# Kernel optimization log

Measured on AMD Instinct MI355X. Metric: run time of the kernel, lower is better.

## Reference

```python
import jax, jax.numpy as jnp
import numpy as np

E = 1024  # dim_model
H = 16    # num_heads
HD = E // H
B, S = 32, 2048
LN_EPS = 1e-5


def setup_inputs() -> dict:
    key = jax.random.key(0)
    ks = jax.random.split(key, 8)
    x = jax.random.normal(ks[0], (B, S, E), dtype=jnp.float32)
    key_padding_mask = jax.random.randint(ks[1], (B, S), 0, 2).astype(jnp.int32)
    # learned seed (xavier_uniform over [1,1,E])
    bound = float(np.sqrt(6.0 / (1 + E)))
    seed = jax.random.uniform(ks[2], (1, 1, E), minval=-bound, maxval=bound, dtype=jnp.float32)
    # MHA params: packed in_proj [3E, E] (q,k,v stacked) + bias, out_proj [E,E]+bias
    w_scale = 1.0 / np.sqrt(E)
    in_proj_w = jax.random.uniform(ks[3], (3 * E, E), minval=-w_scale, maxval=w_scale, dtype=jnp.float32)
    in_proj_b = jnp.zeros((3 * E,), dtype=jnp.float32)
    out_w = jax.random.uniform(ks[4], (E, E), minval=-w_scale, maxval=w_scale, dtype=jnp.float32)
    out_b = jnp.zeros((E,), dtype=jnp.float32)
    ln_g = jnp.ones((E,), dtype=jnp.float32)
    ln_b = jnp.zeros((E,), dtype=jnp.float32)
    return {"x": x, "key_padding_mask": key_padding_mask, "seed": seed,
            "in_proj_w": in_proj_w, "in_proj_b": in_proj_b,
            "out_w": out_w, "out_b": out_b, "ln_g": ln_g, "ln_b": ln_b}


def reference(x, key_padding_mask, seed, in_proj_w, in_proj_b, out_w, out_b, ln_g, ln_b):
    wq, wk, wv = in_proj_w[:E], in_proj_w[E:2 * E], in_proj_w[2 * E:]
    bq, bk, bv = in_proj_b[:E], in_proj_b[E:2 * E], in_proj_b[2 * E:]
    # q from single learned seed: [1,1,E] -> [1,H,1,HD] (broadcast over batch)
    q = (seed @ wq.T + bq).reshape(1, 1, H, HD).transpose(0, 2, 1, 3)
    k = (x @ wk.T + bk).reshape(x.shape[0], -1, H, HD).transpose(0, 2, 1, 3)  # [B,H,S,HD]
    v = (x @ wv.T + bv).reshape(x.shape[0], -1, H, HD).transpose(0, 2, 1, 3)
    scale = 1.0 / jnp.sqrt(jnp.asarray(HD, dtype=x.dtype))
    scores = jnp.einsum('bhqd,bhkd->bhqk', q * scale, k)  # broadcasts q batch dim -> [B,H,1,S]
    pad = (key_padding_mask == 0)[:, None, None, :]  # True = pad
    scores = jnp.where(pad, -jnp.inf, scores)
    attn = jax.nn.softmax(scores, axis=-1)
    ctx = jnp.einsum('bhqk,bhkd->bhqd', attn, v)  # [B,H,1,HD]
    ctx = ctx.transpose(0, 2, 1, 3).reshape(x.shape[0], E)  # squeeze single query
    out = ctx @ out_w.T + out_b
    mu = jnp.mean(out, axis=-1, keepdims=True)
    var = jnp.mean(jnp.square(out - mu), axis=-1, keepdims=True)
    return (out - mu) / jnp.sqrt(var + LN_EPS) * ln_g + ln_b
```

## Files before the change

kernel.cpp:

```cpp
#include <hip/hip_runtime.h>
#include <hip/hip_bf16.h>
#include <math.h>

#define E 1024
#define H 16
#define HD 64
#define B 32
#define S 2048
#define CH 16
#define CTOK (S / CH)
#define SUB 32
#define NSUB (CTOK / SUB)
#define BHE (B * H * E)

typedef __attribute__((ext_vector_type(8))) short short8;
typedef __attribute__((ext_vector_type(4))) float f32x4;

__device__ __forceinline__ short f2bf(float f) {
    union { __hip_bfloat16 h; short s; } u;
    u.h = __float2bfloat16(f);
    return u.s;
}
__device__ __forceinline__ unsigned pack_bf2(float x, float y) {
    unsigned ux = (__float_as_uint(x) + 0x8000u) >> 16;
    unsigned uy = (__float_as_uint(y) + 0x8000u) & 0xffff0000u;
    return uy | ux;
}

__global__ __launch_bounds__(256) void qproj_kernel(const float* __restrict__ W,
                                                    const float* __restrict__ bqkv,
                                                    const float* __restrict__ seed,
                                                    float* __restrict__ q) {
    int gw = (blockIdx.x * 256 + threadIdx.x) >> 6;
    int lane = threadIdx.x & 63;
    if (gw >= E) return;
    const float4* row = (const float4*)(W + (size_t)gw * E);
    const float4* sd = (const float4*)seed;
    float acc = 0.f;
#pragma unroll
    for (int k = 0; k < 4; ++k) {
        float4 w4 = row[k * 64 + lane];
        float4 s4 = sd[k * 64 + lane];
        acc = fmaf(w4.x, s4.x, acc); acc = fmaf(w4.y, s4.y, acc);
        acc = fmaf(w4.z, s4.z, acc); acc = fmaf(w4.w, s4.w, acc);
    }
#pragma unroll
    for (int off = 32; off > 0; off >>= 1) acc += __shfl_down(acc, off, 64);
    if (lane == 0) q[gw] = acc + bqkv[gw];
}

__global__ __launch_bounds__(256) void uproj_kernel(const float* __restrict__ W,
                                                    const float* __restrict__ q,
                                                    short* __restrict__ ubf) {
    int h = blockIdx.y;
    int e = blockIdx.x * 256 + threadIdx.x;
    __shared__ float qs[HD];
    if (threadIdx.x < HD) qs[threadIdx.x] = q[h * HD + threadIdx.x];
    __syncthreads();
    const float* Wk = W + ((size_t)(E + h * HD)) * E + e;
    float acc = 0.f;
#pragma unroll 8
    for (int d = 0; d < HD; ++d) acc = fmaf(qs[d], Wk[(size_t)d * E], acc);
    ubf[(size_t)h * E + e] = f2bf(acc * 0.125f);
}

__global__ __launch_bounds__(512, 4) void fused_kernel(const float* __restrict__ x,
                                                       const int* __restrict__ mask,
                                                       const short* __restrict__ ubf,
                                                       unsigned* __restrict__ partu,
                                                       float* __restrict__ mstat,
                                                       float* __restrict__ lstat) {
    int ss = blockIdx.x, b = blockIdx.y;
    __shared__ short xB[SUB * E];
    __shared__ float scp[8 * 64 * 4];
    __shared__ float pcur[SUB * H];
    __shared__ int   mk[CTOK];
    __shared__ float mrun[H], lrun[H], rfac[H];
    __shared__ float wred[8][16];

    int tid = threadIdx.x, lane = tid & 63, wid = tid >> 6;

    if (tid < H) { mrun[tid] = -1e30f; lrun[tid] = 0.f; }
    for (int i = tid; i < CTOK; i += 512) mk[i] = mask[(size_t)b * S + ss * CTOK + i];

    float4 a4[8];
#pragma unroll
    for (int h = 0; h < 8; ++h) a4[h] = make_float4(0.f, 0.f, 0.f, 0.f);

    int pe4 = tid & 255, phg = tid >> 8;

    __syncthreads();

    for (int sub = 0; sub < NSUB; ++sub) {
        int t0 = sub * SUB;

        {
            int tok = tid >> 4;
            int es  = tid & 15;
            const float* xr = x + ((size_t)b * S + ss * CTOK + t0 + tok) * E;
            bool live = mk[t0 + tok] != 0;
#pragma unroll
            for (int i = 0; i < 8; ++i) {
                int e0 = (es + i * 16) * 8;
                if (live) {
                    float4 lo = *(const float4*)(xr + e0);
                    float4 hi = *(const float4*)(xr + e0 + 4);
                    short8 v;
                    v[0] = f2bf(lo.x); v[1] = f2bf(lo.y); v[2] = f2bf(lo.z); v[3] = f2bf(lo.w);
                    v[4] = f2bf(hi.x); v[5] = f2bf(hi.y); v[6] = f2bf(hi.z); v[7] = f2bf(hi.w);
                    int byte = (tok * 2048 + e0 * 2) ^ ((tok & 7) << 4);
                    *(short8*)((char*)xB + byte) = v;
                }
            }
        }
        __syncthreads();

        {
            int tw = wid & 1, kq = wid >> 1;
            int tr = lane & 15, kg = lane >> 4;
            int tok = tw * 16 + tr;
            f32x4 acc = {0.f, 0.f, 0.f, 0.f};
            const short* ub = ubf + (size_t)tr * E;
#pragma unroll
            for (int st = 0; st < 8; ++st) {
                int e0 = kq * 256 + st * 32 + kg * 8;
                int byte = (tok * 2048 + e0 * 2) ^ ((tok & 7) << 4);
                short8 a = *(const short8*)((char*)xB + byte);
                short8 bv = *(const short8*)(ub + e0);
                acc = __builtin_amdgcn_mfma_f32_16x16x32_bf16(a, bv, acc, 0, 0, 0);
            }
            *(f32x4*)&scp[(wid * 64 + lane) * 4] = acc;
        }
        __syncthreads();

        {
            int tok = tid >> 4, h = tid & 15;
            int tw = tok >> 4, r = tok & 3, kg2 = (tok & 15) >> 2;
            float s = 0.f;
#pragma unroll
            for (int kq = 0; kq < 4; ++kq)
                s += scp[((kq * 2 + tw) * 64 + kg2 * 16 + h) * 4 + r];
            bool live = mk[t0 + tok] != 0;
            float sv = live ? s : -1e30f;
            float mx = sv;
            mx = fmaxf(mx, __shfl_xor(mx, 16, 64));
            mx = fmaxf(mx, __shfl_xor(mx, 32, 64));
            if (lane < 16) wred[wid][lane] = mx;
            __syncthreads();
            if (tid < 16) {
                float mt = wred[0][tid];
#pragma unroll
                for (int w = 1; w < 8; ++w) mt = fmaxf(mt, wred[w][tid]);
                float mo = mrun[tid];
                float mn = fmaxf(mo, mt);
                rfac[tid] = __expf(mo - mn);
                mrun[tid] = mn;
            }
            __syncthreads();
            float p = live ? __expf(s - mrun[h]) : 0.f;
            pcur[tok * 16 + h] = p;
            float ps = p;
            ps += __shfl_xor(ps, 16, 64);
            ps += __shfl_xor(ps, 32, 64);
            if (lane < 16) wred[wid][lane] = ps;
            __syncthreads();
            if (tid < 16) {
                float lt = 0.f;
#pragma unroll
                for (int w = 0; w < 8; ++w) lt += wred[w][tid];
                lrun[tid] = lrun[tid] * rfac[tid] + lt;
            }
        }
        __syncthreads();

        {
            const float* rf = rfac + phg * 8;
#pragma unroll
            for (int h = 0; h < 8; ++h) {
                float r = rf[h];
                a4[h].x *= r; a4[h].y *= r; a4[h].z *= r; a4[h].w *= r;
            }
            int ebyte = pe4 * 8;
            for (int tok = 0; tok < SUB; ++tok) {
                if (!mk[t0 + tok]) continue;
                int byte = (tok * 2048 + ebyte) ^ ((tok & 7) << 4);
                uint2 xv = *(const uint2*)((char*)xB + byte);
                float xe0 = __uint_as_float(xv.x << 16);
                float xe1 = __uint_as_float(xv.x & 0xffff0000u);
                float xe2 = __uint_as_float(xv.y << 16);
                float xe3 = __uint_as_float(xv.y & 0xffff0000u);
                float4 p0 = *(const float4*)&pcur[tok * 16 + phg * 8];
                float4 p1 = *(const float4*)&pcur[tok * 16 + phg * 8 + 4];
                a4[0].x = fmaf(p0.x, xe0, a4[0].x); a4[0].y = fmaf(p0.x, xe1, a4[0].y);
                a4[0].z = fmaf(p0.x, xe2, a4[0].z); a4[0].w = fmaf(p0.x, xe3, a4[0].w);
                a4[1].x = fmaf(p0.y, xe0, a4[1].x); a4[1].y = fmaf(p0.y, xe1, a4[1].y);
                a4[1].z = fmaf(p0.y, xe2, a4[1].z); a4[1].w = fmaf(p0.y, xe3, a4[1].w);
                a4[2].x = fmaf(p0.z, xe0, a4[2].x); a4[2].y = fmaf(p0.z, xe1, a4[2].y);
                a4[2].z = fmaf(p0.z, xe2, a4[2].z); a4[2].w = fmaf(p0.z, xe3, a4[2].w);
                a4[3].x = fmaf(p0.w, xe0, a4[3].x); a4[3].y = fmaf(p0.w, xe1, a4[3].y);
                a4[3].z = fmaf(p0.w, xe2, a4[3].z); a4[3].w = fmaf(p0.w, xe3, a4[3].w);
                a4[4].x = fmaf(p1.x, xe0, a4[4].x); a4[4].y = fmaf(p1.x, xe1, a4[4].y);
                a4[4].z = fmaf(p1.x, xe2, a4[4].z); a4[4].w = fmaf(p1.x, xe3, a4[4].w);
                a4[5].x = fmaf(p1.y, xe0, a4[5].x); a4[5].y = fmaf(p1.y, xe1, a4[5].y);
                a4[5].z = fmaf(p1.y, xe2, a4[5].z); a4[5].w = fmaf(p1.y, xe3, a4[5].w);
                a4[6].x = fmaf(p1.z, xe0, a4[6].x); a4[6].y = fmaf(p1.z, xe1, a4[6].y);
                a4[6].z = fmaf(p1.z, xe2, a4[6].z); a4[6].w = fmaf(p1.z, xe3, a4[6].w);
                a4[7].x = fmaf(p1.w, xe0, a4[7].x); a4[7].y = fmaf(p1.w, xe1, a4[7].y);
                a4[7].z = fmaf(p1.w, xe2, a4[7].z); a4[7].w = fmaf(p1.w, xe3, a4[7].w);
            }
        }
        __syncthreads();
    }

    unsigned* pb = partu + ((size_t)ss * B + b) * (H * E / 2) + pe4 * 2;
#pragma unroll
    for (int h = 0; h < 8; ++h) {
        uint2 v;
        v.x = pack_bf2(a4[h].x, a4[h].y);
        v.y = pack_bf2(a4[h].z, a4[h].w);
        *(uint2*)&pb[(size_t)(phg * 8 + h) * (E / 2)] = v;
    }
    if (tid < 16) {
        mstat[((size_t)ss * B + b) * H + tid] = mrun[tid];
        lstat[((size_t)ss * B + b) * H + tid] = lrun[tid];
    }
}

__global__ __launch_bounds__(256) void ctxc_kernel(const float* __restrict__ W,
                                                   const float* __restrict__ bqkv,
                                                   const unsigned* __restrict__ partu,
                                                   const float* __restrict__ mstat,
                                                   const float* __restrict__ lstat,
                                                   float* __restrict__ ctx) {
    int cb = blockIdx.x, b = blockIdx.y, t = threadIdx.x;
    int h0 = cb * 4;
    __shared__ float xls[4 * E];
    __shared__ float fs[4][CH];
    __shared__ float linv[4];
    if (t < 4) {
        int h = h0 + t;
        float mv[CH];
        float mg = -1e30f;
#pragma unroll
        for (int c = 0; c < CH; ++c) {
            mv[c] = mstat[((size_t)c * B + b) * H + h];
            mg = fmaxf(mg, mv[c]);
        }
        float l = 0.f;
#pragma unroll
        for (int c = 0; c < CH; ++c) {
            float fc = __expf(mv[c] - mg);
            fs[t][c] = fc;
            l = fmaf(fc, lstat[((size_t)c * B + b) * H + h], l);
        }
        linv[t] = 1.f / l;
    }
    __syncthreads();
    for (int i = t; i < 4 * E / 2; i += 256) {
        int hl = i >> 9, e2 = i & 511;
        float sx = 0.f, sy = 0.f;
#pragma unroll 4
        for (int c = 0; c < CH; ++c) {
            float fc = fs[hl][c];
            unsigned v = partu[(((size_t)c * B + b) * H + h0 + hl) * (E / 2) + e2];
            sx = fmaf(fc, __uint_as_float(v << 16), sx);
            sy = fmaf(fc, __uint_as_float(v & 0xffff0000u), sy);
        }
        float li = linv[hl];
        xls[hl * E + e2 * 2] = sx * li;
        xls[hl * E + e2 * 2 + 1] = sy * li;
    }
    __syncthreads();
    int c = cb * 256 + t;
    int h = c >> 6;
    const float4* wr = (const float4*)(W + ((size_t)(2 * E + c)) * E);
    const float4* xl = (const float4*)(xls + (h - h0) * E);
    float acc = bqkv[2 * E + c];
#pragma unroll 4
    for (int e4 = 0; e4 < E / 4; ++e4) {
        float4 w = wr[e4], xv = xl[e4];
        acc = fmaf(w.x, xv.x, acc); acc = fmaf(w.y, xv.y, acc);
        acc = fmaf(w.z, xv.z, acc); acc = fmaf(w.w, xv.w, acc);
    }
    ctx[(size_t)b * E + c] = acc;
}

__global__ __launch_bounds__(256) void outproj_kernel(const float* __restrict__ Wo,
                                                      const float* __restrict__ ob,
                                                      const float* __restrict__ ctx,
                                                      float* __restrict__ outpre) {
    int obk = blockIdx.x, b = blockIdx.y, t = threadIdx.x;
    int o = obk * 256 + t;
    __shared__ float cl[E];
    const float4* cp = (const float4*)(ctx + (size_t)b * E);
    for (int i = t; i < E / 4; i += 256) ((float4*)cl)[i] = cp[i];
    __syncthreads();
    const float4* wr = (const float4*)(Wo + (size_t)o * E);
    const float4* cl4 = (const float4*)cl;
    float acc = ob[o];
#pragma unroll 4
    for (int e4 = 0; e4 < E / 4; ++e4) {
        float4 w = wr[e4], cv = cl4[e4];
        acc = fmaf(w.x, cv.x, acc); acc = fmaf(w.y, cv.y, acc);
        acc = fmaf(w.z, cv.z, acc); acc = fmaf(w.w, cv.w, acc);
    }
    outpre[(size_t)b * E + o] = acc;
}

__global__ __launch_bounds__(256) void ln_kernel(const float* __restrict__ outpre,
                                                 const float* __restrict__ g,
                                                 const float* __restrict__ bb,
                                                 float* __restrict__ out) {
    int b = blockIdx.x, t = threadIdx.x, lane = t & 63, wid = t >> 6;
    const float4* row = (const float4*)(outpre + (size_t)b * E);
    float4 v = row[t];
    float s = v.x + v.y + v.z + v.w;
    float sq = v.x * v.x + v.y * v.y + v.z * v.z + v.w * v.w;
    __shared__ float rs[4], rq[4];
#pragma unroll
    for (int off = 32; off > 0; off >>= 1) {
        s += __shfl_down(s, off, 64);
        sq += __shfl_down(sq, off, 64);
    }
    if (lane == 0) { rs[wid] = s; rq[wid] = sq; }
    __syncthreads();
    s = rs[0] + rs[1] + rs[2] + rs[3];
    sq = rq[0] + rq[1] + rq[2] + rq[3];
    float mean = s * (1.f / E);
    float var = sq * (1.f / E) - mean * mean;
    float inv = rsqrtf(var + 1e-5f);
    float4 gv = ((const float4*)g)[t];
    float4 bv = ((const float4*)bb)[t];
    float4 o;
    o.x = (v.x - mean) * inv * gv.x + bv.x;
    o.y = (v.y - mean) * inv * gv.y + bv.y;
    o.z = (v.z - mean) * inv * gv.z + bv.z;
    o.w = (v.w - mean) * inv * gv.w + bv.w;
    ((float4*)(out + (size_t)b * E))[t] = o;
}

extern "C" void kernel_launch(void* const* d_in, const int* in_sizes, int n_in,
                              void* d_out, int out_size, void* d_ws, size_t ws_size,
                              hipStream_t stream) {
    const float* x    = (const float*)d_in[0];
    const int*   mask = (const int*)d_in[1];
    const float* seed = (const float*)d_in[2];
    const float* W    = (const float*)d_in[3];
    const float* bqkv = (const float*)d_in[4];
    const float* Wo   = (const float*)d_in[5];
    const float* ob   = (const float*)d_in[6];
    const float* g    = (const float*)d_in[7];
    const float* lb   = (const float*)d_in[8];
    float* out = (float*)d_out;

    float* ws = (float*)d_ws;
    float* q        = ws;
    unsigned* partu = (unsigned*)(q + E);
    float* mstat    = (float*)(partu + (size_t)CH * BHE / 2);
    float* lstat    = mstat + (size_t)CH * B * H;
    short* ubf      = (short*)(lstat + (size_t)CH * B * H);
    float* ctx      = (float*)(ubf + (size_t)H * E);
    float* outpre   = ctx + (size_t)B * E;

    qproj_kernel<<<256, 256, 0, stream>>>(W, bqkv, seed, q);
    uproj_kernel<<<dim3(E / 256, H), 256, 0, stream>>>(W, q, ubf);
    fused_kernel<<<dim3(CH, B), 512, 0, stream>>>(x, mask, ubf, partu, mstat, lstat);
    ctxc_kernel<<<dim3(E / 256, B), 256, 0, stream>>>(W, bqkv, partu, mstat, lstat, ctx);
    outproj_kernel<<<dim3(E / 256, B), 256, 0, stream>>>(Wo, ob, ctx, outpre);
    ln_kernel<<<B, 256, 0, stream>>>(outpre, g, lb, out);
}
```

Before: 132.4 us.

## Double sequence chunks, halve fused-kernel block size, widen per-thread pooling accumulators

```diff
diff --git a/kernel.cpp b/kernel.cpp
--- a/kernel.cpp
+++ b/kernel.cpp
@@ -7,9 +7,9 @@
 #define HD 64
 #define B 32
 #define S 2048
-#define CH 16
+#define CH 32
 #define CTOK (S / CH)
-#define SUB 32
+#define SUB 16
 #define NSUB (CTOK / SUB)
 #define BHE (B * H * E)
 
@@ -64,7 +64,7 @@
     ubf[(size_t)h * E + e] = f2bf(acc * 0.125f);
 }
 
-__global__ __launch_bounds__(512, 4) void fused_kernel(const float* __restrict__ x,
+__global__ __launch_bounds__(256, 4) void fused_kernel(const float* __restrict__ x,
                                                        const int* __restrict__ mask,
                                                        const short* __restrict__ ubf,
                                                        unsigned* __restrict__ partu,
@@ -72,22 +72,25 @@
                                                        float* __restrict__ lstat) {
     int ss = blockIdx.x, b = blockIdx.y;
     __shared__ short xB[SUB * E];
-    __shared__ float scp[8 * 64 * 4];
+    __shared__ float scp[4 * 64 * 4];
     __shared__ float pcur[SUB * H];
     __shared__ int   mk[CTOK];
     __shared__ float mrun[H], lrun[H], rfac[H];
-    __shared__ float wred[8][16];
+    __shared__ float wred[4][16];
 
     int tid = threadIdx.x, lane = tid & 63, wid = tid >> 6;
 
     if (tid < H) { mrun[tid] = -1e30f; lrun[tid] = 0.f; }
-    for (int i = tid; i < CTOK; i += 512) mk[i] = mask[(size_t)b * S + ss * CTOK + i];
-
-    float4 a4[8];
-#pragma unroll
-    for (int h = 0; h < 8; ++h) a4[h] = make_float4(0.f, 0.f, 0.f, 0.f);
-
-    int pe4 = tid & 255, phg = tid >> 8;
+    if (tid < CTOK) mk[tid] = mask[(size_t)b * S + ss * CTOK + tid];
+
+    int e8 = tid & 127;
+    int hg = tid >> 7;
+    float4 accA[8], accB[8];
+#pragma unroll
+    for (int h = 0; h < 8; ++h) {
+        accA[h] = make_float4(0.f, 0.f, 0.f, 0.f);
+        accB[h] = make_float4(0.f, 0.f, 0.f, 0.f);
+    }
 
     __syncthreads();
 
@@ -116,9 +119,9 @@
         __syncthreads();
 
         {
-            int tw = wid & 1, kq = wid >> 1;
+            int kq = wid;
             int tr = lane & 15, kg = lane >> 4;
-            int tok = tw * 16 + tr;
+            int tok = tr;
             f32x4 acc = {0.f, 0.f, 0.f, 0.f};
             const short* ub = ubf + (size_t)tr * E;
 #pragma unroll
@@ -135,11 +138,11 @@
 
         {
             int tok = tid >> 4, h = tid & 15;
-            int tw = tok >> 4, r = tok & 3, kg2 = (tok & 15) >> 2;
+            int r = tok & 3, kg2 = tok >> 2;
             float s = 0.f;
 #pragma unroll
             for (int kq = 0; kq < 4; ++kq)
-                s += scp[((kq * 2 + tw) * 64 + kg2 * 16 + h) * 4 + r];
+                s += scp[((kq * 4 + kg2) * 16 + h) * 4 + r];
             bool live = mk[t0 + tok] != 0;
             float sv = live ? s : -1e30f;
             float mx = sv;
@@ -150,7 +153,7 @@
             if (tid < 16) {
                 float mt = wred[0][tid];
 #pragma unroll
-                for (int w = 1; w < 8; ++w) mt = fmaxf(mt, wred[w][tid]);
+                for (int w = 1; w < 4; ++w) mt = fmaxf(mt, wred[w][tid]);
                 float mo = mrun[tid];
                 float mn = fmaxf(mo, mt);
                 rfac[tid] = __expf(mo - mn);
@@ -167,58 +170,63 @@
             if (tid < 16) {
                 float lt = 0.f;
 #pragma unroll
-                for (int w = 0; w < 8; ++w) lt += wred[w][tid];
+                for (int w = 0; w < 4; ++w) lt += wred[w][tid];
                 lrun[tid] = lrun[tid] * rfac[tid] + lt;
             }
         }
         __syncthreads();
 
         {
-            const float* rf = rfac + phg * 8;
+            const float* rf = rfac + hg * 8;
 #pragma unroll
             for (int h = 0; h < 8; ++h) {
                 float r = rf[h];
-                a4[h].x *= r; a4[h].y *= r; a4[h].z *= r; a4[h].w *= r;
-            }
-            int ebyte = pe4 * 8;
+                accA[h].x *= r; accA[h].y *= r; accA[h].z *= r; accA[h].w *= r;
+                accB[h].x *= r; accB[h].y *= r; accB[h].z *= r; accB[h].w *= r;
+            }
+            int ebyte = e8 * 16;
             for (int tok = 0; tok < SUB; ++tok) {
                 if (!mk[t0 + tok]) continue;
                 int byte = (tok * 2048 + ebyte) ^ ((tok & 7) << 4);
-                uint2 xv = *(const uint2*)((char*)xB + byte);
+                uint4 xv = *(const uint4*)((char*)xB + byte);
                 float xe0 = __uint_as_float(xv.x << 16);
                 float xe1 = __uint_as_float(xv.x & 0xffff0000u);
                 float xe2 = __uint_as_float(xv.y << 16);
                 float xe3 = __uint_as_float(xv.y & 0xffff0000u);
-                float4 p0 = *(const float4*)&pcur[tok * 16 + phg * 8];
-                float4 p1 = *(const float4*)&pcur[tok * 16 + phg * 8 + 4];
-                a4[0].x = fmaf(p0.x, xe0, a4[0].x); a4[0].y = fmaf(p0.x, xe1, a4[0].y);
-                a4[0].z = fmaf(p0.x, xe2, a4[0].z); a4[0].w = fmaf(p0.x, xe3, a4[0].w);
-                a4[1].x = fmaf(p0.y, xe0, a4[1].x); a4[1].y = fmaf(p0.y, xe1, a4[1].y);
-                a4[1].z = fmaf(p0.y, xe2, a4[1].z); a4[1].w = fmaf(p0.y, xe3, a4[1].w);
-                a4[2].x = fmaf(p0.z, xe0, a4[2].x); a4[2].y = fmaf(p0.z, xe1, a4[2].y);
-                a4[2].z = fmaf(p0.z, xe2, a4[2].z); a4[2].w = fmaf(p0.z, xe3, a4[2].w);
-                a4[3].x = fmaf(p0.w, xe0, a4[3].x); a4[3].y = fmaf(p0.w, xe1, a4[3].y);
-                a4[3].z = fmaf(p0.w, xe2, a4[3].z); a4[3].w = fmaf(p0.w, xe3, a4[3].w);
-                a4[4].x = fmaf(p1.x, xe0, a4[4].x); a4[4].y = fmaf(p1.x, xe1, a4[4].y);
-                a4[4].z = fmaf(p1.x, xe2, a4[4].z); a4[4].w = fmaf(p1.x, xe3, a4[4].w);
-                a4[5].x = fmaf(p1.y, xe0, a4[5].x); a4[5].y = fmaf(p1.y, xe1, a4[5].y);
-                a4[5].z = fmaf(p1.y, xe2, a4[5].z); a4[5].w = fmaf(p1.y, xe3, a4[5].w);
-                a4[6].x = fmaf(p1.z, xe0, a4[6].x); a4[6].y = fmaf(p1.z, xe1, a4[6].y);
-                a4[6].z = fmaf(p1.z, xe2, a4[6].z); a4[6].w = fmaf(p1.z, xe3, a4[6].w);
-                a4[7].x = fmaf(p1.w, xe0, a4[7].x); a4[7].y = fmaf(p1.w, xe1, a4[7].y);
-                a4[7].z = fmaf(p1.w, xe2, a4[7].z); a4[7].w = fmaf(p1.w, xe3, a4[7].w);
+                float xe4 = __uint_as_float(xv.z << 16);
+                float xe5 = __uint_as_float(xv.z & 0xffff0000u);
+                float xe6 = __uint_as_float(xv.w << 16);
+                float xe7 = __uint_as_float(xv.w & 0xffff0000u);
+                float4 p0 = *(const float4*)&pcur[tok * 16 + hg * 8];
+                float4 p1 = *(const float4*)&pcur[tok * 16 + hg * 8 + 4];
+#define POOLH(A, Bv, P) \
+                A.x = fmaf(P, xe0, A.x); A.y = fmaf(P, xe1, A.y); \
+                A.z = fmaf(P, xe2, A.z); A.w = fmaf(P, xe3, A.w); \
+                Bv.x = fmaf(P, xe4, Bv.x); Bv.y = fmaf(P, xe5, Bv.y); \
+                Bv.z = fmaf(P, xe6, Bv.z); Bv.w = fmaf(P, xe7, Bv.w);
+                POOLH(accA[0], accB[0], p0.x)
+                POOLH(accA[1], accB[1], p0.y)
+                POOLH(accA[2], accB[2], p0.z)
+                POOLH(accA[3], accB[3], p0.w)
+                POOLH(accA[4], accB[4], p1.x)
+                POOLH(accA[5], accB[5], p1.y)
+                POOLH(accA[6], accB[6], p1.z)
+                POOLH(accA[7], accB[7], p1.w)
+#undef POOLH
             }
         }
         __syncthreads();
     }
 
-    unsigned* pb = partu + ((size_t)ss * B + b) * (H * E / 2) + pe4 * 2;
+    unsigned* pb = partu + ((size_t)ss * B + b) * (H * E / 2) + e8 * 4;
 #pragma unroll
     for (int h = 0; h < 8; ++h) {
-        uint2 v;
-        v.x = pack_bf2(a4[h].x, a4[h].y);
-        v.y = pack_bf2(a4[h].z, a4[h].w);
-        *(uint2*)&pb[(size_t)(phg * 8 + h) * (E / 2)] = v;
+        uint4 v;
+        v.x = pack_bf2(accA[h].x, accA[h].y);
+        v.y = pack_bf2(accA[h].z, accA[h].w);
+        v.z = pack_bf2(accB[h].x, accB[h].y);
+        v.w = pack_bf2(accB[h].z, accB[h].w);
+        *(uint4*)&pb[(size_t)(hg * 8 + h) * (E / 2)] = v;
     }
     if (tid < 16) {
         mstat[((size_t)ss * B + b) * H + tid] = mrun[tid];
@@ -364,7 +372,7 @@
 
     qproj_kernel<<<256, 256, 0, stream>>>(W, bqkv, seed, q);
     uproj_kernel<<<dim3(E / 256, H), 256, 0, stream>>>(W, q, ubf);
-    fused_kernel<<<dim3(CH, B), 512, 0, stream>>>(x, mask, ubf, partu, mstat, lstat);
+    fused_kernel<<<dim3(CH, B), 256, 0, stream>>>(x, mask, ubf, partu, mstat, lstat);
     ctxc_kernel<<<dim3(E / 256, B), 256, 0, stream>>>(W, bqkv, partu, mstat, lstat, ctx);
     outproj_kernel<<<dim3(E / 256, B), 256, 0, stream>>>(Wo, ob, ctx, outpre);
     ln_kernel<<<B, 256, 0, stream>>>(outpre, g, lb, out);
```

New measurement: 159.0 us. +20.1%, slower.
